# Kernel tuning notes

Hardware: AMD Instinct MI355X
Metric: run time of the kernel (lower is better)

## Reference

```python
import jax, jax.numpy as jnp
import numpy as np

NFIELD, NKER = 8, 16
B, Y, X, P, T = 32, 32, 32, 16, 8


def setup_inputs() -> dict:
    key = jax.random.key(0)
    k1, k2 = jax.random.split(key)
    fieldpatch = jax.random.normal(k1, (B, NFIELD, Y, X, P, T), dtype=jnp.float32)
    quadpatch = jax.random.uniform(k2, (B, Y, X, P, T), dtype=jnp.float32)
    zeros_fk = jnp.zeros((NFIELD, NKER), dtype=jnp.float32)
    return {
        "fieldpatch": fieldpatch,
        "quadpatch": quadpatch,
        "mean_lat": zeros_fk, "logstd_lat": zeros_fk,
        "mean_lon": zeros_fk, "logstd_lon": zeros_fk,
        "mean_lev": zeros_fk, "logstd_lev": zeros_fk,
        "logtau_time": zeros_fk,
    }


def _gaussian1d(mean, logstd, length):
    # (f, k, length): exp(-0.5*((coord - mean)/std)^2), coord in [-1, 1]
    coord = jnp.linspace(-1.0, 1.0, length, dtype=mean.dtype)
    std = jnp.exp(logstd)
    z = (coord[None, None, :] - mean[..., None]) / std[..., None]
    return jnp.exp(-0.5 * z * z)


def _exponential1d(logtau, length):
    # (f, k, length): exp(-coord / tau), coord = 0..length-1
    coord = jnp.arange(length, dtype=logtau.dtype)
    tau = jnp.exp(logtau) + 1e-4
    return jnp.exp(-coord[None, None, :] / tau[..., None])


def reference(fieldpatch, quadpatch, mean_lat, logstd_lat, mean_lon, logstd_lon,
              mean_lev, logstd_lev, logtau_time):
    b, f, y, x, p, t = fieldpatch.shape
    ky = _gaussian1d(mean_lat, logstd_lat, y)      # (f,k,y)
    kx = _gaussian1d(mean_lon, logstd_lon, x)      # (f,k,x)
    kp = _gaussian1d(mean_lev, logstd_lev, p)      # (f,k,p)
    kt = _exponential1d(logtau_time, t)            # (f,k,t)
    # Separable outer product -> full kernel (f,k,y,x,p,t)
    kernel = jnp.einsum('fky,fkx,fkp,fkt->fkyxpt', ky, kx, kp, kt)
    qmean = quadpatch.mean(axis=0)                 # (y,x,p,t)
    integral = jnp.einsum('fkyxpt,yxpt->fk', kernel, qmean) + 1e-4
    weights = kernel / integral[:, :, None, None, None, None]
    # torch weights() runs under @torch.no_grad(): weights are constant wrt autograd
    weights = jax.lax.stop_gradient(weights)
    features = jnp.einsum('bfyxpt,fkyxpt,byxpt->bfk', fieldpatch, weights, quadpatch)
    return features.reshape(b, -1)
```

## Files before the change

kernel.cpp:

```cpp
#include <hip/hip_runtime.h>
#include <math.h>

#define NF 8
#define NK 16
#define BB 32
#define YY 32
#define XX 32
#define PP 16
#define TT 8
#define YX (YY*XX)
#define PT (PP*TT)
#define YXPT (YX*PT)
#define CHUNKS 8
#define COLS_PER_BLOCK (YX/CHUNKS)
#define COLS_PER_WAVE  (COLS_PER_BLOCK/4)
#define MAIN_ITERS     (COLS_PER_WAVE/2)

#define WPT_OFF   0
#define WYX_OFF   (NF*NK*PT)
#define QMEAN_OFF (WYX_OFF + NF*YX*NK)
#define ACC_OFF   (QMEAN_OFF + YXPT)
#define INTG_OFF  (ACC_OFF + BB*NF*NK)

__global__ __launch_bounds__(256) void k_prep(const float* __restrict__ quad,
                       const float* __restrict__ mean_lat, const float* __restrict__ logstd_lat,
                       const float* __restrict__ mean_lon, const float* __restrict__ logstd_lon,
                       const float* __restrict__ mean_lev, const float* __restrict__ logstd_lev,
                       const float* __restrict__ logtau,
                       float* __restrict__ ws) {
    const int tid = threadIdx.x, bx = blockIdx.x;

    if (bx < 512) {
        __shared__ float4 sm[256];
        const int j4 = bx * 64 + (tid & 63);
        const int bg = tid >> 6;
        const float4* q4 = (const float4*)quad;
        float4 a = make_float4(0.f, 0.f, 0.f, 0.f);
        #pragma unroll
        for (int i = 0; i < 8; ++i) {
            float4 v = q4[(size_t)(bg * 8 + i) * (YXPT / 4) + j4];
            a.x += v.x; a.y += v.y; a.z += v.z; a.w += v.w;
        }
        sm[tid] = a;
        __syncthreads();
        if (tid < 64) {
            float4 r0 = sm[tid], r1 = sm[tid + 64], r2 = sm[tid + 128], r3 = sm[tid + 192];
            float4 r;
            r.x = (r0.x + r1.x + r2.x + r3.x) * (1.f / BB);
            r.y = (r0.y + r1.y + r2.y + r3.y) * (1.f / BB);
            r.z = (r0.z + r1.z + r2.z + r3.z) * (1.f / BB);
            r.w = (r0.w + r1.w + r2.w + r3.w) * (1.f / BB);
            ((float4*)(ws + QMEAN_OFF))[j4] = r;
        }
        return;
    }
    if (bx == 640) {
        for (int i = tid; i < BB * NF * NK; i += 256) ws[ACC_OFF + i] = 0.f;
        if (tid < NF * NK) ws[INTG_OFF + tid] = 1e-4f;
        return;
    }
    const int fk = bx - 512;
    if (tid >= 128) return;
    const int f = fk >> 4, k = fk & 15;
    const float mlat = mean_lat[fk], slat = expf(logstd_lat[fk]);
    const float mlon = mean_lon[fk], slon = expf(logstd_lon[fk]);
    const float mlev = mean_lev[fk], slev = expf(logstd_lev[fk]);
    const float tau  = expf(logtau[fk]) + 1e-4f;

    {
        const int p = tid >> 3, t = tid & 7;
        const float cp = -1.f + 2.f * (float)p / (PP - 1);
        const float zp = (cp - mlev) / slev;
        ws[WPT_OFF + fk * PT + tid] = expf(-0.5f * zp * zp) * expf(-(float)t / tau);
    }
    #pragma unroll
    for (int i = 0; i < 8; ++i) {
        const int yx = i * 128 + tid;
        const int y = yx >> 5, x = yx & 31;
        const float cy = -1.f + 2.f * (float)y / (YY - 1);
        const float cx = -1.f + 2.f * (float)x / (XX - 1);
        const float zy = (cy - mlat) / slat;
        const float zx = (cx - mlon) / slon;
        ws[WYX_OFF + (f * YX + yx) * NK + k] = expf(-0.5f * zy * zy) * expf(-0.5f * zx * zx);
    }
}

__global__ __launch_bounds__(256) void k_integral(float* __restrict__ ws) {
    const int fk = blockIdx.x >> 2, qr = blockIdx.x & 3;
    const int tid = threadIdx.x;
    const int f = fk >> 4, k = fk & 15;
    const int yx = qr * 256 + tid;
    const float4* w4 = (const float4*)(ws + WPT_OFF + fk * PT);
    const float4* q4 = (const float4*)(ws + QMEAN_OFF + (size_t)yx * PT);
    float s = 0.f;
    #pragma unroll
    for (int j = 0; j < PT / 4; ++j) {
        float4 w = w4[j], q = q4[j];
        s += w.x * q.x + w.y * q.y + w.z * q.z + w.w * q.w;
    }
    float partial = ws[WYX_OFF + (f * YX + yx) * NK + k] * s;
    #pragma unroll
    for (int m = 32; m; m >>= 1) partial += __shfl_xor(partial, m);
    __shared__ float red[4];
    if ((tid & 63) == 0) red[tid >> 6] = partial;
    __syncthreads();
    if (tid == 0) atomicAdd(ws + INTG_OFF + fk, red[0] + red[1] + red[2] + red[3]);
}

__global__ __launch_bounds__(256, 4) void k_main(const float* __restrict__ field,
                                                 const float* __restrict__ quad,
                                                 float* __restrict__ ws) {
    const int bx = blockIdx.x;
    const int f = bx & 7, chunk = (bx >> 3) & 7, b = bx >> 6;
    const int tid = threadIdx.x;
    const int wave = tid >> 6, L = tid & 63;
    const int half = L >> 5, qg = L & 31;

    float4 wf[NK];
    #pragma unroll
    for (int k = 0; k < NK; ++k)
        wf[k] = *(const float4*)(ws + WPT_OFF + (f * NK + k) * PT + 4 * qg);

    float acc[NK];
    #pragma unroll
    for (int k = 0; k < NK; ++k) acc[k] = 0.f;

    const int colBase = chunk * COLS_PER_BLOCK + wave * COLS_PER_WAVE;
    const float* fptr = field + (size_t)(b * NF + f) * YXPT + colBase * PT + 4 * L;
    const float* qptr = quad + (size_t)b * YXPT + colBase * PT + 4 * L;
    const float* wyxc = ws + WYX_OFF + (f * YX + colBase + half) * NK;

    #pragma unroll 2
    for (int s = 0; s < MAIN_ITERS; ++s) {
        float4 fv = *(const float4*)(fptr + s * 2 * PT);
        float4 qv = *(const float4*)(qptr + s * 2 * PT);
        const float4* wy = (const float4*)(wyxc + s * 2 * NK);
        float4 a0 = wy[0], a1 = wy[1], a2 = wy[2], a3 = wy[3];
        float wv[NK];
        *(float4*)(wv + 0)  = a0;
        *(float4*)(wv + 4)  = a1;
        *(float4*)(wv + 8)  = a2;
        *(float4*)(wv + 12) = a3;
        float4 g;
        g.x = fv.x * qv.x; g.y = fv.y * qv.y; g.z = fv.z * qv.z; g.w = fv.w * qv.w;
        #pragma unroll
        for (int k = 0; k < NK; ++k) {
            float d = g.x * wf[k].x;
            d = fmaf(g.y, wf[k].y, d);
            d = fmaf(g.z, wf[k].z, d);
            d = fmaf(g.w, wf[k].w, d);
            acc[k] = fmaf(wv[k], d, acc[k]);
        }
    }

    __shared__ float red[4][NK];
    #pragma unroll
    for (int k = 0; k < NK; ++k) {
        float v = acc[k];
        v += __shfl_xor(v, 32); v += __shfl_xor(v, 16); v += __shfl_xor(v, 8);
        v += __shfl_xor(v, 4);  v += __shfl_xor(v, 2);  v += __shfl_xor(v, 1);
        if (L == 0) red[wave][k] = v;
    }
    __syncthreads();
    if (tid < NK) {
        float s2 = red[0][tid] + red[1][tid] + red[2][tid] + red[3][tid];
        atomicAdd(ws + ACC_OFF + (b * NF + f) * NK + tid, s2);
    }
}

__global__ void k_final(const float* __restrict__ ws, float* __restrict__ out) {
    int i = blockIdx.x * 256 + threadIdx.x;
    if (i < BB * NF * NK)
        out[i] = ws[ACC_OFF + i] / ws[INTG_OFF + (i & (NF * NK - 1))];
}

extern "C" void kernel_launch(void* const* d_in, const int* in_sizes, int n_in,
                              void* d_out, int out_size, void* d_ws, size_t ws_size,
                              hipStream_t stream) {
    const float* field = (const float*)d_in[0];
    const float* quad  = (const float*)d_in[1];
    float* ws = (float*)d_ws;

    k_prep<<<641, 256, 0, stream>>>(quad,
        (const float*)d_in[2], (const float*)d_in[3],
        (const float*)d_in[4], (const float*)d_in[5],
        (const float*)d_in[6], (const float*)d_in[7],
        (const float*)d_in[8], ws);
    k_integral<<<NF * NK * 4, 256, 0, stream>>>(ws);
    k_main<<<BB * NF * CHUNKS, 256, 0, stream>>>(field, quad, ws);
    k_final<<<(BB * NF * NK + 255) / 256, 256, 0, stream>>>(ws, (float*)d_out);
}
```

Measured before the change: 268.9 us.

## Stage spatial weights in LDS, prefetch loads, replace atomics with partial buffers

The main kernel now copies each block's slice of the yx weights into shared memory and reads them from there. Field and quad loads are software-pipelined two steps ahead, and the field loads are marked nontemporal. The atomic accumulations in the integral and main kernels become plain stores into per-chunk and per-quarter partial buffers, which the final kernel sums, so the zeroing block in prep goes away. The aim is to cut redundant global weight traffic and to hide load latency, at the cost of more registers, extra shared memory and a larger workspace.

```diff
diff --git a/kernel.cpp b/kernel.cpp
--- a/kernel.cpp
+++ b/kernel.cpp
@@ -16,11 +16,13 @@
 #define COLS_PER_WAVE  (COLS_PER_BLOCK/4)
 #define MAIN_ITERS     (COLS_PER_WAVE/2)
 
+typedef float vf4 __attribute__((ext_vector_type(4)));
+
 #define WPT_OFF   0
 #define WYX_OFF   (NF*NK*PT)
 #define QMEAN_OFF (WYX_OFF + NF*YX*NK)
 #define ACC_OFF   (QMEAN_OFF + YXPT)
-#define INTG_OFF  (ACC_OFF + BB*NF*NK)
+#define INTG_OFF  (ACC_OFF + CHUNKS*BB*NF*NK)
 
 __global__ __launch_bounds__(256) void k_prep(const float* __restrict__ quad,
                        const float* __restrict__ mean_lat, const float* __restrict__ logstd_lat,
@@ -54,11 +56,6 @@
         }
         return;
     }
-    if (bx == 640) {
-        for (int i = tid; i < BB * NF * NK; i += 256) ws[ACC_OFF + i] = 0.f;
-        if (tid < NF * NK) ws[INTG_OFF + tid] = 1e-4f;
-        return;
-    }
     const int fk = bx - 512;
     if (tid >= 128) return;
     const int f = fk >> 4, k = fk & 15;
@@ -104,7 +101,8 @@
     __shared__ float red[4];
     if ((tid & 63) == 0) red[tid >> 6] = partial;
     __syncthreads();
-    if (tid == 0) atomicAdd(ws + INTG_OFF + fk, red[0] + red[1] + red[2] + red[3]);
+    if (tid == 0)
+        ws[INTG_OFF + qr * (NF * NK) + fk] = red[0] + red[1] + red[2] + red[3];
 }
 
 __global__ __launch_bounds__(256, 4) void k_main(const float* __restrict__ field,
@@ -116,6 +114,14 @@
     const int wave = tid >> 6, L = tid & 63;
     const int half = L >> 5, qg = L & 31;
 
+    __shared__ float sw[COLS_PER_BLOCK * NK];
+    {
+        const float4* src = (const float4*)(ws + WYX_OFF + (size_t)(f * YX + chunk * COLS_PER_BLOCK) * NK);
+        float4* dst = (float4*)sw;
+        dst[tid] = src[tid];
+        dst[tid + 256] = src[tid + 256];
+    }
+
     float4 wf[NK];
     #pragma unroll
     for (int k = 0; k < NK; ++k)
@@ -126,30 +132,66 @@
     for (int k = 0; k < NK; ++k) acc[k] = 0.f;
 
     const int colBase = chunk * COLS_PER_BLOCK + wave * COLS_PER_WAVE;
-    const float* fptr = field + (size_t)(b * NF + f) * YXPT + colBase * PT + 4 * L;
-    const float* qptr = quad + (size_t)b * YXPT + colBase * PT + 4 * L;
-    const float* wyxc = ws + WYX_OFF + (f * YX + colBase + half) * NK;
-
-    #pragma unroll 2
+    const vf4* fp = (const vf4*)(field + (size_t)(b * NF + f) * YXPT + (size_t)colBase * PT + 4 * L);
+    const vf4* qp = (const vf4*)(quad + (size_t)b * YXPT + (size_t)colBase * PT + 4 * L);
+    const int STEP = (2 * PT) / 4;
+
+    __syncthreads();
+    const float* swc = sw + (wave * COLS_PER_WAVE + half) * NK;
+
+    vf4 fa = __builtin_nontemporal_load(fp);
+    vf4 qa = qp[0];
+    vf4 fb = __builtin_nontemporal_load(fp + STEP);
+    vf4 qb = qp[STEP];
+    vf4 ga = fa * qa;
+
+    #pragma unroll
     for (int s = 0; s < MAIN_ITERS; ++s) {
-        float4 fv = *(const float4*)(fptr + s * 2 * PT);
-        float4 qv = *(const float4*)(qptr + s * 2 * PT);
-        const float4* wy = (const float4*)(wyxc + s * 2 * NK);
-        float4 a0 = wy[0], a1 = wy[1], a2 = wy[2], a3 = wy[3];
-        float wv[NK];
-        *(float4*)(wv + 0)  = a0;
-        *(float4*)(wv + 4)  = a1;
-        *(float4*)(wv + 8)  = a2;
-        *(float4*)(wv + 12) = a3;
-        float4 g;
-        g.x = fv.x * qv.x; g.y = fv.y * qv.y; g.z = fv.z * qv.z; g.w = fv.w * qv.w;
+        vf4 fc = fb, qc = qb;
+        if (s + 2 < MAIN_ITERS) {
+            fc = __builtin_nontemporal_load(fp + (s + 2) * STEP);
+            qc = qp[(s + 2) * STEP];
+        }
+        const float4* wvp = (const float4*)(swc + s * 2 * NK);
         #pragma unroll
-        for (int k = 0; k < NK; ++k) {
-            float d = g.x * wf[k].x;
-            d = fmaf(g.y, wf[k].y, d);
-            d = fmaf(g.z, wf[k].z, d);
-            d = fmaf(g.w, wf[k].w, d);
-            acc[k] = fmaf(wv[k], d, acc[k]);
+        for (int j = 0; j < 4; ++j) {
+            float4 w = wvp[j];
+            {
+                const int k = 4 * j;
+                float d = ga.x * wf[k].x;
+                d = fmaf(ga.y, wf[k].y, d);
+                d = fmaf(ga.z, wf[k].z, d);
+                d = fmaf(ga.w, wf[k].w, d);
+                acc[k] = fmaf(w.x, d, acc[k]);
+            }
+            {
+                const int k = 4 * j + 1;
+                float d = ga.x * wf[k].x;
+                d = fmaf(ga.y, wf[k].y, d);
+                d = fmaf(ga.z, wf[k].z, d);
+                d = fmaf(ga.w, wf[k].w, d);
+                acc[k] = fmaf(w.y, d, acc[k]);
+            }
+            {
+                const int k = 4 * j + 2;
+                float d = ga.x * wf[k].x;
+                d = fmaf(ga.y, wf[k].y, d);
+                d = fmaf(ga.z, wf[k].z, d);
+                d = fmaf(ga.w, wf[k].w, d);
+                acc[k] = fmaf(w.z, d, acc[k]);
+            }
+            {
+                const int k = 4 * j + 3;
+                float d = ga.x * wf[k].x;
+                d = fmaf(ga.y, wf[k].y, d);
+                d = fmaf(ga.z, wf[k].z, d);
+                d = fmaf(ga.w, wf[k].w, d);
+                acc[k] = fmaf(w.w, d, acc[k]);
+            }
+        }
+        if (s + 1 < MAIN_ITERS) {
+            ga = fb * qb;
+            fb = fc; qb = qc;
         }
     }
 
@@ -164,14 +206,21 @@
     __syncthreads();
     if (tid < NK) {
         float s2 = red[0][tid] + red[1][tid] + red[2][tid] + red[3][tid];
-        atomicAdd(ws + ACC_OFF + (b * NF + f) * NK + tid, s2);
+        ws[ACC_OFF + chunk * (BB * NF * NK) + (b * NF + f) * NK + tid] = s2;
     }
 }
 
 __global__ void k_final(const float* __restrict__ ws, float* __restrict__ out) {
     int i = blockIdx.x * 256 + threadIdx.x;
-    if (i < BB * NF * NK)
-        out[i] = ws[ACC_OFF + i] / ws[INTG_OFF + (i & (NF * NK - 1))];
+    if (i >= BB * NF * NK) return;
+    float a = 0.f;
+    #pragma unroll
+    for (int c = 0; c < CHUNKS; ++c) a += ws[ACC_OFF + c * (BB * NF * NK) + i];
+    const int fk = i & (NF * NK - 1);
+    float g = 1e-4f;
+    #pragma unroll
+    for (int q = 0; q < 4; ++q) g += ws[INTG_OFF + q * (NF * NK) + fk];
+    out[i] = a / g;
 }
 
 extern "C" void kernel_launch(void* const* d_in, const int* in_sizes, int n_in,
@@ -181,7 +230,7 @@
     const float* quad  = (const float*)d_in[1];
     float* ws = (float*)d_ws;
 
-    k_prep<<<641, 256, 0, stream>>>(quad,
+    k_prep<<<640, 256, 0, stream>>>(quad,
         (const float*)d_in[2], (const float*)d_in[3],
         (const float*)d_in[4], (const float*)d_in[5],
         (const float*)d_in[6], (const float*)d_in[7],
```

After: 666.5 us. 148% more time.

## Double-buffer field/quad tiles via async global-to-LDS loads, stage weights in LDS

Applied to the files above, without the earlier changes.

The main kernel now stages the per-chunk spatial weights and time/level weights in LDS and streams field and quad tiles into double-buffered LDS using global_load_lds with explicit vmcnt waits, overlapping loads with compute. Atomic accumulation is replaced with per-chunk and per-quarter partial buffers summed in the final kernel, which also removes the zeroing block. This targets memory latency and uncoalesced weight loads, at the cost of higher LDS use and lower occupancy.

```diff
diff --git a/kernel.cpp b/kernel.cpp
--- a/kernel.cpp
+++ b/kernel.cpp
@@ -13,14 +13,15 @@
 #define YXPT (YX*PT)
 #define CHUNKS 8
 #define COLS_PER_BLOCK (YX/CHUNKS)
-#define COLS_PER_WAVE  (COLS_PER_BLOCK/4)
-#define MAIN_ITERS     (COLS_PER_WAVE/2)
+#define TCOLS 16
+#define NTILES (COLS_PER_BLOCK/TCOLS)
+#define TFLOATS (TCOLS*PT)
 
 #define WPT_OFF   0
 #define WYX_OFF   (NF*NK*PT)
 #define QMEAN_OFF (WYX_OFF + NF*YX*NK)
 #define ACC_OFF   (QMEAN_OFF + YXPT)
-#define INTG_OFF  (ACC_OFF + BB*NF*NK)
+#define INTG_OFF  (ACC_OFF + CHUNKS*BB*NF*NK)
 
 __global__ __launch_bounds__(256) void k_prep(const float* __restrict__ quad,
                        const float* __restrict__ mean_lat, const float* __restrict__ logstd_lat,
@@ -54,11 +55,6 @@
         }
         return;
     }
-    if (bx == 640) {
-        for (int i = tid; i < BB * NF * NK; i += 256) ws[ACC_OFF + i] = 0.f;
-        if (tid < NF * NK) ws[INTG_OFF + tid] = 1e-4f;
-        return;
-    }
     const int fk = bx - 512;
     if (tid >= 128) return;
     const int f = fk >> 4, k = fk & 15;
@@ -104,10 +100,18 @@
     __shared__ float red[4];
     if ((tid & 63) == 0) red[tid >> 6] = partial;
     __syncthreads();
-    if (tid == 0) atomicAdd(ws + INTG_OFF + fk, red[0] + red[1] + red[2] + red[3]);
-}
-
-__global__ __launch_bounds__(256, 4) void k_main(const float* __restrict__ field,
+    if (tid == 0)
+        ws[INTG_OFF + qr * (NF * NK) + fk] = red[0] + red[1] + red[2] + red[3];
+}
+
+__device__ __forceinline__ void gld16(const float* g, float* l) {
+    __builtin_amdgcn_global_load_lds(
+        (const __attribute__((address_space(1))) void*)(g),
+        (__attribute__((address_space(3))) void*)(l),
+        16, 0, 0);
+}
+
+__global__ __launch_bounds__(256, 3) void k_main(const float* __restrict__ field,
                                                  const float* __restrict__ quad,
                                                  float* __restrict__ ws) {
     const int bx = blockIdx.x;
@@ -115,63 +119,117 @@
     const int tid = threadIdx.x;
     const int wave = tid >> 6, L = tid & 63;
     const int half = L >> 5, qg = L & 31;
+    const int lofs = 4 * L;
+    const int WSEG = wave * (TFLOATS / 4);
+
+    __shared__ float lds[12288];
+    float* sw   = lds;
+    float* swpt = lds + 2048;
+    float* ft0  = lds + 4096;
+    float* ft1  = lds + 6144;
+    float* qt0  = lds + 8192;
+    float* qt1  = lds + 10240;
+
+    {
+        const float4* srcW = (const float4*)(ws + WYX_OFF + (size_t)(f * YX + chunk * COLS_PER_BLOCK) * NK);
+        ((float4*)sw)[tid]       = srcW[tid];
+        ((float4*)sw)[tid + 256] = srcW[tid + 256];
+        const float4* srcP = (const float4*)(ws + WPT_OFF + (size_t)f * NK * PT);
+        ((float4*)swpt)[tid]       = srcP[tid];
+        ((float4*)swpt)[tid + 256] = srcP[tid + 256];
+    }
+    __syncthreads();
 
     float4 wf[NK];
     #pragma unroll
     for (int k = 0; k < NK; ++k)
-        wf[k] = *(const float4*)(ws + WPT_OFF + (f * NK + k) * PT + 4 * qg);
+        wf[k] = *(const float4*)(swpt + k * PT + 4 * qg);
 
     float acc[NK];
     #pragma unroll
     for (int k = 0; k < NK; ++k) acc[k] = 0.f;
 
-    const int colBase = chunk * COLS_PER_BLOCK + wave * COLS_PER_WAVE;
-    const float* fptr = field + (size_t)(b * NF + f) * YXPT + colBase * PT + 4 * L;
-    const float* qptr = quad + (size_t)b * YXPT + colBase * PT + 4 * L;
-    const float* wyxc = ws + WYX_OFF + (f * YX + colBase + half) * NK;
-
-    #pragma unroll 2
-    for (int s = 0; s < MAIN_ITERS; ++s) {
-        float4 fv = *(const float4*)(fptr + s * 2 * PT);
-        float4 qv = *(const float4*)(qptr + s * 2 * PT);
-        const float4* wy = (const float4*)(wyxc + s * 2 * NK);
-        float4 a0 = wy[0], a1 = wy[1], a2 = wy[2], a3 = wy[3];
-        float wv[NK];
-        *(float4*)(wv + 0)  = a0;
-        *(float4*)(wv + 4)  = a1;
-        *(float4*)(wv + 8)  = a2;
-        *(float4*)(wv + 12) = a3;
-        float4 g;
-        g.x = fv.x * qv.x; g.y = fv.y * qv.y; g.z = fv.z * qv.z; g.w = fv.w * qv.w;
-        #pragma unroll
-        for (int k = 0; k < NK; ++k) {
-            float d = g.x * wf[k].x;
-            d = fmaf(g.y, wf[k].y, d);
-            d = fmaf(g.z, wf[k].z, d);
-            d = fmaf(g.w, wf[k].w, d);
-            acc[k] = fmaf(wv[k], d, acc[k]);
-        }
-    }
-
-    __shared__ float red[4][NK];
+    __syncthreads();
+
+    const float* fgbase = field + (size_t)(b * NF + f) * YXPT + (size_t)(chunk * COLS_PER_BLOCK) * PT;
+    const float* qgbase = quad + (size_t)b * YXPT + (size_t)(chunk * COLS_PER_BLOCK) * PT;
+
+    #define DMA_TILE(t, fb, qb)                                                     \
+        do {                                                                        \
+            gld16(fgbase + (t) * TFLOATS + WSEG + 0 * 256 + lofs, (fb) + WSEG + 0 * 256 + lofs); \
+            gld16(fgbase + (t) * TFLOATS + WSEG + 1 * 256 + lofs, (fb) + WSEG + 1 * 256 + lofs); \
+            gld16(qgbase + (t) * TFLOATS + WSEG + 0 * 256 + lofs, (qb) + WSEG + 0 * 256 + lofs); \
+            gld16(qgbase + (t) * TFLOATS + WSEG + 1 * 256 + lofs, (qb) + WSEG + 1 * 256 + lofs); \
+        } while (0)
+
+    #define COMP_TILE(t, fb, qb)                                                    \
+        do {                                                                        \
+            _Pragma("unroll")                                                       \
+            for (int j = 0; j < 2; ++j) {                                           \
+                float4 fv = *(const float4*)((fb) + WSEG + j * 256 + lofs);         \
+                float4 qv = *(const float4*)((qb) + WSEG + j * 256 + lofs);         \
+                const int c = (t) * TCOLS + wave * 4 + 2 * j + half;                \
+                const float4* wvp = (const float4*)(sw + c * NK);                   \
+                float4 a0 = wvp[0], a1 = wvp[1], a2 = wvp[2], a3 = wvp[3];          \
+                float wv[NK];                                                       \
+                *(float4*)(wv + 0)  = a0;                                           \
+                *(float4*)(wv + 4)  = a1;                                           \
+                *(float4*)(wv + 8)  = a2;                                           \
+                *(float4*)(wv + 12) = a3;                                           \
+                float4 ga;                                                          \
+                ga.x = fv.x * qv.x; ga.y = fv.y * qv.y;                             \
+                ga.z = fv.z * qv.z; ga.w = fv.w * qv.w;                             \
+                _Pragma("unroll")                                                   \
+                for (int k = 0; k < NK; ++k) {                                      \
+                    float d = ga.x * wf[k].x;                                       \
+                    d = fmaf(ga.y, wf[k].y, d);                                     \
+                    d = fmaf(ga.z, wf[k].z, d);                                     \
+                    d = fmaf(ga.w, wf[k].w, d);                                     \
+                    acc[k] = fmaf(wv[k], d, acc[k]);                                \
+                }                                                                   \
+            }                                                                       \
+        } while (0)
+
+    #define WAITV4 asm volatile("s_waitcnt vmcnt(4)" ::: "memory")
+    #define WAITV0 asm volatile("s_waitcnt vmcnt(0)" ::: "memory")
+
+    DMA_TILE(0, ft0, qt0);
+    DMA_TILE(1, ft1, qt1);
+    WAITV4; COMP_TILE(0, ft0, qt0); DMA_TILE(2, ft0, qt0);
+    WAITV4; COMP_TILE(1, ft1, qt1); DMA_TILE(3, ft1, qt1);
+    WAITV4; COMP_TILE(2, ft0, qt0); DMA_TILE(4, ft0, qt0);
+    WAITV4; COMP_TILE(3, ft1, qt1); DMA_TILE(5, ft1, qt1);
+    WAITV4; COMP_TILE(4, ft0, qt0); DMA_TILE(6, ft0, qt0);
+    WAITV4; COMP_TILE(5, ft1, qt1); DMA_TILE(7, ft1, qt1);
+    WAITV4; COMP_TILE(6, ft0, qt0);
+    WAITV0; COMP_TILE(7, ft1, qt1);
+
+    float* red = swpt;
     #pragma unroll
     for (int k = 0; k < NK; ++k) {
         float v = acc[k];
         v += __shfl_xor(v, 32); v += __shfl_xor(v, 16); v += __shfl_xor(v, 8);
         v += __shfl_xor(v, 4);  v += __shfl_xor(v, 2);  v += __shfl_xor(v, 1);
-        if (L == 0) red[wave][k] = v;
+        if (L == 0) red[wave * NK + k] = v;
     }
     __syncthreads();
     if (tid < NK) {
-        float s2 = red[0][tid] + red[1][tid] + red[2][tid] + red[3][tid];
-        atomicAdd(ws + ACC_OFF + (b * NF + f) * NK + tid, s2);
+        float s2 = red[0 * NK + tid] + red[1 * NK + tid] + red[2 * NK + tid] + red[3 * NK + tid];
+        ws[ACC_OFF + chunk * (BB * NF * NK) + (b * NF + f) * NK + tid] = s2;
     }
 }
 
 __global__ void k_final(const float* __restrict__ ws, float* __restrict__ out) {
     int i = blockIdx.x * 256 + threadIdx.x;
-    if (i < BB * NF * NK)
-        out[i] = ws[ACC_OFF + i] / ws[INTG_OFF + (i & (NF * NK - 1))];
+    if (i >= BB * NF * NK) return;
+    float a = 0.f;
+    #pragma unroll
+    for (int c = 0; c < CHUNKS; ++c) a += ws[ACC_OFF + c * (BB * NF * NK) + i];
+    const int fk = i & (NF * NK - 1);
+    float g = 1e-4f;
+    #pragma unroll
+    for (int q = 0; q < 4; ++q) g += ws[INTG_OFF + q * (NF * NK) + fk];
+    out[i] = a / g;
 }
 
 extern "C" void kernel_launch(void* const* d_in, const int* in_sizes, int n_in,
@@ -181,7 +239,7 @@
     const float* quad  = (const float*)d_in[1];
     float* ws = (float*)d_ws;
 
-    k_prep<<<641, 256, 0, stream>>>(quad,
+    k_prep<<<640, 256, 0, stream>>>(quad,
         (const float*)d_in[2], (const float*)d_in[3],
         (const float*)d_in[4], (const float*)d_in[5],
         (const float*)d_in[6], (const float*)d_in[7],
```

Result: slower. 604.6 us (+124.8%).
